# Optimization experiments

Measured on AMD Instinct MI355X. Metric: run time of the kernel, lower is better.

## Reference

```python
import jax, jax.numpy as jnp
import numpy as np

K = 3  # kernel_size

def setup_inputs() -> dict:
    key = jax.random.key(0)
    k1, k2, k3 = jax.random.split(key, 3)
    B, C, H, W = 8, 64, 128, 128
    x = jax.random.normal(k1, (B, C, H, W), dtype=jnp.float32)
    # 1x1 conv weight (out_channels*K*K, in_channels) and bias
    W_gen = jax.random.normal(k2, (C * K * K, C), dtype=jnp.float32) / np.float32(np.sqrt(C))
    b_gen = jax.random.normal(k3, (C * K * K,), dtype=jnp.float32) * 0.01
    return {"x": x, "W_gen": W_gen, "b_gen": b_gen}

def reference(x, W_gen, b_gen):
    B, C, H, W = x.shape  # out_channels == in_channels (required by the view)
    # filter_gen: 1x1 conv + ReLU -> (B, C*K*K, H, W)
    f = jax.nn.relu(jnp.einsum('bchw,oc->bohw', x, W_gen) + b_gen[None, :, None, None])
    filters = f.reshape(B, C, K * K, H, W)
    # F.unfold with padding=(K-1)//2, stride 1: gather KxK patches per pixel.
    pad = (K - 1) // 2
    xp = jnp.pad(x, ((0, 0), (0, 0), (pad, pad), (pad, pad)))
    # kernel-position index runs row-major (i*K + j), matching unfold layout
    patches = jnp.stack([xp[:, :, i:i + H, j:j + W]
                         for i in range(K) for j in range(K)], axis=2)  # (B,C,K*K,H,W)
    out = (filters * patches).sum(axis=2)  # (B,C,H,W)
    return out
```

## Files before the change

kernel.cpp:

```cpp
#include <hip/hip_runtime.h>
#include <hip/hip_bf16.h>

#define CC 64
#define HH 128
#define WW 128
#define OO 576
#define HW (HH * WW)

typedef __attribute__((ext_vector_type(8))) short short8;
typedef __attribute__((ext_vector_type(4))) float floatx4;

__device__ __forceinline__ unsigned short f2bf(float f) {
    unsigned u = __float_as_uint(f);
    u = (u + 0x7FFFu + ((u >> 16) & 1u)) >> 16;
    return (unsigned short)u;
}

__global__ void ACDA_wconv_kernel(const float* __restrict__ Wg,
                                  unsigned short* __restrict__ Wb) {
    int i = blockIdx.x * 256 + threadIdx.x;
    if (i < OO * CC) Wb[i] = f2bf(Wg[i]);
}

__global__ __launch_bounds__(64) void ACDA_main_kernel(
    const float* __restrict__ x, const unsigned short* __restrict__ Wb,
    const float* __restrict__ bg, float* __restrict__ out)
{
    __shared__ float Fbuf[16][68];

    const int lane = threadIdx.x;
    const int quad = lane >> 4;
    const int l16  = lane & 15;

    const int bid = blockIdx.x;
    const int wv  = bid & 3;
    const int seg = (bid >> 2) & 1;
    const int h   = (bid >> 3) & 127;
    const int b   = bid >> 10;
    const int w0  = seg << 6;

    const float* xb = x + (size_t)b * CC * HW;

    short8 bfrag[4][2];
#pragma unroll
    for (int nt = 0; nt < 4; ++nt) {
#pragma unroll
        for (int ks = 0; ks < 2; ++ks) {
            short8 v;
            const int w = w0 + nt * 16 + l16;
#pragma unroll
            for (int j = 0; j < 8; j += 2) {
                const int c = ks * 32 + quad * 8 + j;
                float f0 = xb[(c * HH + h) * WW + w];
                float f1 = xb[((c + 1) * HH + h) * WW + w];
                __hip_bfloat162 p = __float22bfloat162_rn(make_float2(f0, f1));
                unsigned u;
                __builtin_memcpy(&u, &p, 4);
                v[j]     = (short)(u & 0xffffu);
                v[j + 1] = (short)(u >> 16);
            }
            bfrag[nt][ks] = v;
        }
    }

    int wA = w0 + lane - 1; bool badA = (wA < 0);   if (badA) wA = 0;
    int wB = w0 + lane;
    int wC = w0 + lane + 1; bool badC = (wC > 127); if (badC) wC = 127;
    int rt[3]; bool rbad[3];
#pragma unroll
    for (int di = 0; di < 3; ++di) {
        int rr = h + di - 1;
        rbad[di] = (rr < 0) || (rr > 127);
        rr = rr < 0 ? 0 : (rr > 127 ? 127 : rr);
        rt[di] = rr * WW;
    }
    const int wsel[3]  = {wA, wB, wC};
    const bool wbad[3] = {badA, false, badC};
    const int soffC = wv * 16 * HW;
    int  pb[3][3]; bool bad[3][3];
#pragma unroll
    for (int di = 0; di < 3; ++di)
#pragma unroll
        for (int dj = 0; dj < 3; ++dj) {
            pb[di][dj]  = soffC + rt[di] + wsel[dj];
            bad[di][dj] = rbad[di] || wbad[dj];
        }

    float oacc[16];
#pragma unroll
    for (int i = 0; i < 16; ++i) oacc[i] = 0.f;

#pragma unroll
    for (int t = 0; t < 9; ++t) {
        const int obase = wv * 144 + t * 16;
        const unsigned short* wrow = Wb + (obase + l16) * CC + quad * 8;
        short8 a0 = *(const short8*)(wrow);
        short8 a1 = *(const short8*)(wrow + 32);
        floatx4 acc[4];
#pragma unroll
        for (int nt = 0; nt < 4; ++nt) {
            floatx4 z = {0.f, 0.f, 0.f, 0.f};
            z = __builtin_amdgcn_mfma_f32_16x16x32_bf16(a0, bfrag[nt][0], z, 0, 0, 0);
            z = __builtin_amdgcn_mfma_f32_16x16x32_bf16(a1, bfrag[nt][1], z, 0, 0, 0);
            acc[nt] = z;
        }
#pragma unroll
        for (int nt = 0; nt < 4; ++nt)
#pragma unroll
            for (int reg = 0; reg < 4; ++reg)
                Fbuf[quad * 4 + reg][nt * 16 + l16] = acc[nt][reg];

        __syncthreads();

#pragma unroll
        for (int r = 0; r < 16; ++r) {
            const int idx   = t * 16 + r;
            const int c_rel = idx / 9;
            const int kk    = idx - 9 * c_rel;
            const int di    = kk / 3;
            const int dj    = kk - 3 * di;
            float fv = Fbuf[r][lane] + bg[obase + r];
            fv = fmaxf(fv, 0.f);
            float pv = xb[pb[di][dj] + c_rel * HW];
            if (bad[di][dj]) pv = 0.f;
            oacc[c_rel] = fmaf(fv, pv, oacc[c_rel]);
        }
    }

    float* ob = out + (size_t)b * CC * HW + h * WW + w0 + lane;
#pragma unroll
    for (int i = 0; i < 16; ++i)
        ob[(wv * 16 + i) * HW] = oacc[i];
}

extern "C" void kernel_launch(void* const* d_in, const int* in_sizes, int n_in,
                              void* d_out, int out_size, void* d_ws, size_t ws_size,
                              hipStream_t stream) {
    const float* x  = (const float*)d_in[0];
    const float* Wg = (const float*)d_in[1];
    const float* bg = (const float*)d_in[2];
    float* out = (float*)d_out;
    unsigned short* Wb = (unsigned short*)d_ws;

    ACDA_wconv_kernel<<<dim3((OO * CC + 255) / 256), dim3(256), 0, stream>>>(Wg, Wb);
    ACDA_main_kernel<<<dim3(8 * 128 * 2 * 4), dim3(64), 0, stream>>>(x, Wb, bg, out);
}
```

Baseline: 120.3 us.

## Pack four waves per block, transpose LDS filter buffer, drop barrier

Merges the four per-wave blocks into one 256-thread block that covers a 64-pixel row segment, and swizzles block IDs. Each wave now writes its MFMA results into a private transposed LDS slice with vector stores and reads them back as float4. Because each wave reads only its own slice, the __syncthreads is removed. This cuts scalar LDS traffic and barrier cost, and lets the x-loads of the sibling waves share cache, at the price of a larger shared footprint and more register pressure under the new launch bounds.

```diff
diff --git a/kernel.cpp b/kernel.cpp
--- a/kernel.cpp
+++ b/kernel.cpp
@@ -22,21 +22,23 @@
     if (i < OO * CC) Wb[i] = f2bf(Wg[i]);
 }
 
-__global__ __launch_bounds__(64) void ACDA_main_kernel(
+__global__ __launch_bounds__(256, 8) void ACDA_main_kernel(
     const float* __restrict__ x, const unsigned short* __restrict__ Wb,
     const float* __restrict__ bg, float* __restrict__ out)
 {
-    __shared__ float Fbuf[16][68];
+    __shared__ float FbufT[4][64][20];
 
-    const int lane = threadIdx.x;
+    const int tid  = threadIdx.x;
+    const int lane = tid & 63;
+    const int wv   = tid >> 6;
     const int quad = lane >> 4;
     const int l16  = lane & 15;
 
     const int bid = blockIdx.x;
-    const int wv  = bid & 3;
-    const int seg = (bid >> 2) & 1;
-    const int h   = (bid >> 3) & 127;
-    const int b   = bid >> 10;
+    const int wk  = (bid & 7) * 256 + (bid >> 3);
+    const int seg = wk & 1;
+    const int h   = (wk >> 1) & 127;
+    const int b   = wk >> 8;
     const int w0  = seg << 6;
 
     const float* xb = x + (size_t)b * CC * HW;
@@ -96,34 +98,31 @@
         const unsigned short* wrow = Wb + (obase + l16) * CC + quad * 8;
         short8 a0 = *(const short8*)(wrow);
         short8 a1 = *(const short8*)(wrow + 32);
-        floatx4 acc[4];
 #pragma unroll
         for (int nt = 0; nt < 4; ++nt) {
             floatx4 z = {0.f, 0.f, 0.f, 0.f};
             z = __builtin_amdgcn_mfma_f32_16x16x32_bf16(a0, bfrag[nt][0], z, 0, 0, 0);
             z = __builtin_amdgcn_mfma_f32_16x16x32_bf16(a1, bfrag[nt][1], z, 0, 0, 0);
-            acc[nt] = z;
+            *(floatx4*)&FbufT[wv][nt * 16 + l16][quad * 4] = z;
         }
-#pragma unroll
-        for (int nt = 0; nt < 4; ++nt)
-#pragma unroll
-            for (int reg = 0; reg < 4; ++reg)
-                Fbuf[quad * 4 + reg][nt * 16 + l16] = acc[nt][reg];
-
-        __syncthreads();
 
 #pragma unroll
-        for (int r = 0; r < 16; ++r) {
-            const int idx   = t * 16 + r;
-            const int c_rel = idx / 9;
-            const int kk    = idx - 9 * c_rel;
-            const int di    = kk / 3;
-            const int dj    = kk - 3 * di;
-            float fv = Fbuf[r][lane] + bg[obase + r];
-            fv = fmaxf(fv, 0.f);
-            float pv = xb[pb[di][dj] + c_rel * HW];
-            if (bad[di][dj]) pv = 0.f;
-            oacc[c_rel] = fmaf(fv, pv, oacc[c_rel]);
+        for (int g = 0; g < 4; ++g) {
+            floatx4 f4 = *(const floatx4*)&FbufT[wv][lane][g * 4];
+#pragma unroll
+            for (int rr = 0; rr < 4; ++rr) {
+                const int r     = g * 4 + rr;
+                const int idx   = t * 16 + r;
+                const int c_rel = idx / 9;
+                const int kk    = idx - 9 * c_rel;
+                const int di    = kk / 3;
+                const int dj    = kk - 3 * di;
+                float fv = f4[rr] + bg[obase + r];
+                fv = fmaxf(fv, 0.f);
+                float pv = xb[pb[di][dj] + c_rel * HW];
+                if (bad[di][dj]) pv = 0.f;
+                oacc[c_rel] = fmaf(fv, pv, oacc[c_rel]);
+            }
         }
     }
 
@@ -143,5 +142,5 @@
     unsigned short* Wb = (unsigned short*)d_ws;
 
     ACDA_wconv_kernel<<<dim3((OO * CC + 255) / 256), dim3(256), 0, stream>>>(Wg, Wb);
-    ACDA_main_kernel<<<dim3(8 * 128 * 2 * 4), dim3(64), 0, stream>>>(x, Wb, bg, out);
+    ACDA_main_kernel<<<dim3(8 * 128 * 2), dim3(256), 0, stream>>>(x, Wb, bg, out);
 }
```

After: 252.8 us. +110.1%, slower.
